# Kernel tuning notes

Hardware: AMD Instinct MI355X
Metric: run time of the kernel (lower is better)

## Reference

```python
import jax, jax.numpy as jnp
import numpy as np

C = 128        # in_channels
HEADS = 4
B, D, H, W = 4, 16, 64, 64  # H must equal W for this module's matmul to type-check


def conv1x1(x, Wm, b):
    # 1x1x1 Conv3d == per-voxel linear over channels
    return jnp.einsum('bcdhw,oc->bodhw', x, Wm) + b[None, :, None, None, None]


def setup_inputs() -> dict:
    key = jax.random.key(0)
    ks = jax.random.split(key, 14)
    scale = 1.0 / np.sqrt(C)

    def wmat(k):
        return jax.random.normal(k, (C, C), jnp.float32) * scale

    def bvec(k):
        return jax.random.normal(k, (C,), jnp.float32) * 0.01

    return {
        'x':  jax.random.normal(ks[0], (B, C, D, H, W), jnp.float32),
        'Wq': wmat(ks[1]),  'bq': bvec(ks[2]),
        'Wk': wmat(ks[3]),  'bk': bvec(ks[4]),
        'Wv': wmat(ks[5]),  'bv': bvec(ks[6]),
        'Wa1': wmat(ks[7]), 'ba1': bvec(ks[8]),
        'Wa2': wmat(ks[9]), 'ba2': bvec(ks[10]),
        'Wf': wmat(ks[11]), 'bf': bvec(ks[12]),
    }


def reference(x, Wq, bq, Wk, bk, Wv, bv, Wa1, ba1, Wa2, ba2, Wf, bf):
    b, c, d, h, w = x.shape
    ch = c // HEADS  # channels per head

    q = conv1x1(x, Wq, bq).reshape(b, HEADS, ch, d, h, w)
    k = conv1x1(x, Wk, bk).reshape(b, HEADS, ch, d, h, w)
    v = conv1x1(x, Wv, bv).reshape(b, HEADS, ch, d, h, w)

    # attention over the last spatial axis: (W, H)^T @ (H, W) -> (W, W)
    attn = jnp.einsum('bhcdxi,bhcdxj->bhcdij', q, k)  # [b, heads, ch, d, W, W]
    attn = jax.nn.softmax(attn, axis=-1)
    # (W, W) @ (H=W, W) -> (W, W)
    out = jnp.einsum('bhcdik,bhcdkj->bhcdij', attn, v)
    out = out.reshape(b, c, d, h, w)

    # depth=1 attention layer: conv1x1 -> relu -> conv1x1
    out = conv1x1(jax.nn.relu(conv1x1(out, Wa1, ba1)), Wa2, ba2)
    out = conv1x1(out, Wf, bf)
    return out
```

## Files before the change

kernel.cpp:

```cpp
#include <hip/hip_runtime.h>


#define CCH 128
#define SPB 65536
#define NBATCH 4
#define WTAB 16384
#define TSZ  16384

typedef float f32x4 __attribute__((ext_vector_type(4)));
typedef __bf16 bf16x8 __attribute__((ext_vector_type(8)));
typedef short s16x8 __attribute__((ext_vector_type(8)));
typedef unsigned short u16x8 __attribute__((ext_vector_type(8)));
typedef unsigned short u16x4 __attribute__((ext_vector_type(4)));
typedef unsigned int u32x2 __attribute__((ext_vector_type(2)));

template <typename T>
static __device__ __forceinline__ auto mfma_try(T a, T b, f32x4 c, int)
    -> decltype(__builtin_amdgcn_mfma_f32_16x16x32_bf16(a, b, c, 0, 0, 0)) {
  return __builtin_amdgcn_mfma_f32_16x16x32_bf16(a, b, c, 0, 0, 0);
}
template <typename T>
static __device__ __forceinline__ f32x4 mfma_try(T a, T b, f32x4 c, long) {
  return __builtin_amdgcn_mfma_f32_16x16x32_bf16(
      __builtin_bit_cast(bf16x8, a), __builtin_bit_cast(bf16x8, b), c, 0, 0, 0);
}
static __device__ __forceinline__ f32x4 MFMA16(u16x8 a, u16x8 b, f32x4 c) {
  return mfma_try(__builtin_bit_cast(s16x8, a), __builtin_bit_cast(s16x8, b), c, 0);
}

static __device__ __forceinline__ unsigned short f2b(float f) {
  return __builtin_bit_cast(unsigned short, (__bf16)f);
}
static __device__ __forceinline__ unsigned int pk2(float a, float b) {
  return (unsigned int)f2b(a) | ((unsigned int)f2b(b) << 16);
}

static __device__ __forceinline__ void glds16(const unsigned short* g,
                                              unsigned short* l) {
  __builtin_amdgcn_global_load_lds(
      (const __attribute__((address_space(1))) unsigned int*)g,
      (__attribute__((address_space(3))) unsigned int*)l, 16, 0, 0);
}

static __device__ __forceinline__ void bar_lgkm() {
  asm volatile("s_waitcnt lgkmcnt(0)" ::: "memory");
  __builtin_amdgcn_sched_barrier(0);
  __builtin_amdgcn_s_barrier();
  __builtin_amdgcn_sched_barrier(0);
}
static __device__ __forceinline__ void bar_vm0() {
  asm volatile("s_waitcnt vmcnt(0)" ::: "memory");
  __builtin_amdgcn_sched_barrier(0);
  __builtin_amdgcn_s_barrier();
  __builtin_amdgcn_sched_barrier(0);
}

static __device__ __forceinline__ int swzc(int r, int c) {
  int slot = ((c >> 3) ^ (r & 7) ^ ((r >> 3) & 15)) & 15;
  return r * 128 + slot * 8 + (c & 7);
}
static __device__ __forceinline__ int widx(int r, int c) {
  return (r & 64) * 128 + swzc(r & 63, c);
}
static __device__ __forceinline__ int swat(int w, int x) {
  int slot = ((x >> 3) ^ (w & 7) ^ ((w >> 3) & 7)) & 7;
  return w * 64 + slot * 8 + (x & 7);
}
static __device__ __forceinline__ int pix(int i, int j) {
  int slot = ((j >> 3) ^ (((i >> 2) & 3) << 1)) & 7;
  return i * 64 + slot * 8 + (j & 7);
}
static __device__ __forceinline__ int fdx(int o, int slot) {
  return o * 128 + ((slot ^ ((o & 7) << 2)) & 31) * 4;
}

__global__ __launch_bounds__(256) void prep_w_kernel(
    const float* __restrict__ Wq, const float* __restrict__ Wk,
    const float* __restrict__ Wv, const float* __restrict__ W1,
    const float* __restrict__ W2, const float* __restrict__ W3,
    unsigned short* __restrict__ out)
{
  const float* Ws[6] = {Wq, Wk, Wv, W1, W2, W3};
  const float* W = Ws[blockIdx.x];
  unsigned short* o = out + (size_t)blockIdx.x * WTAB;
  const int tid = threadIdx.x;
#pragma unroll
  for (int p = 0; p < 16; ++p) {
    const int base = p * 1024 + tid * 4;
    const int m = base >> 7;
    const int c0 = base & 127;
    f32x4 v = *(const f32x4*)&W[base];
    u16x4 u;
#pragma unroll
    for (int e = 0; e < 4; ++e) u[e] = f2b(v[e]);
    *(u16x4*)&o[widx(m, c0)] = u;
  }
}

__global__ __launch_bounds__(512, 2) void qkv_kernel(
    const float* __restrict__ X, const unsigned short* __restrict__ Wbf,
    const float* __restrict__ Bq, const float* __restrict__ Bk,
    const float* __restrict__ Bv,
    unsigned short* __restrict__ Yq, unsigned short* __restrict__ Yk,
    unsigned short* __restrict__ Yv)
{
  __shared__ unsigned short wt[3 * WTAB];
  __shared__ unsigned short xb[WTAB];

  const int tid  = threadIdx.x;
  const int wv   = tid >> 6;
  const int lane = tid & 63;
  const int lr   = lane & 15;
  const int lg   = lane >> 4;
  const int sw   = wv >> 2;
  const int ow   = wv & 3;
  const int lin  = blockIdx.x;
  const int swz  = ((lin & 7) << 6) | (lin >> 3);
  const int sbase = (swz & 127) * 512;
  const size_t xoff = (size_t)(swz >> 7) * CCH * SPB;
  const int go = tid * 8;

#pragma unroll
  for (int t = 0; t < 3; ++t)
#pragma unroll
    for (int p = 0; p < 4; ++p)
      glds16(&Wbf[t * WTAB + p * 4096 + go], &wt[t * WTAB + p * 4096 + go]);

  float bias_r[3][2];
#pragma unroll
  for (int of = 0; of < 2; ++of) {
    bias_r[0][of] = Bq[ow * 32 + of * 16 + lr];
    bias_r[1][of] = Bk[ow * 32 + of * 16 + lr];
    bias_r[2][of] = Bv[ow * 32 + of * 16 + lr];
  }

  const int c0  = (tid >> 3) * 2;
  const int sb8 = (tid & 7) * 4;
  const float* xrow = X + xoff + (size_t)c0 * SPB + sbase;
  unsigned int* xb32 = (unsigned int*)xb;

  f32x4 xr[8];
#pragma unroll
  for (int i = 0; i < 4; ++i) {
    xr[i]     = *(const f32x4*)&xrow[sb8 + 32 * i];
    xr[4 + i] = *(const f32x4*)&xrow[SPB + sb8 + 32 * i];
  }
#pragma unroll
  for (int i = 0; i < 4; ++i)
#pragma unroll
    for (int e = 0; e < 4; ++e)
      xb32[swzc(sb8 + 32 * i + e, c0) >> 1] = pk2(xr[i][e], xr[4 + i][e]);
  __syncthreads();

#pragma unroll
  for (int si = 0; si < 4; ++si) {
    const size_t yb =
        ((size_t)(swz >> 7) * 512 + (size_t)(swz & 127) * 4 + si) * TSZ;

    if (si < 3) {
      const float* xn = xrow + (si + 1) * 128;
#pragma unroll
      for (int i = 0; i < 4; ++i) {
        xr[i]     = *(const f32x4*)&xn[sb8 + 32 * i];
        xr[4 + i] = *(const f32x4*)&xn[SPB + sb8 + 32 * i];
      }
    }
    u16x8 afr[4][4];
#pragma unroll
    for (int sf = 0; sf < 4; ++sf)
#pragma unroll
      for (int ks = 0; ks < 4; ++ks)
        afr[sf][ks] = *(const u16x8*)
            &xb[swzc(sw * 64 + sf * 16 + lr, ks * 32 + lg * 8)];
    bar_lgkm();

    auto conv = [&](int t, unsigned short* __restrict__ Y) {
      f32x4 acc[4][2];
#pragma unroll
      for (int sf = 0; sf < 4; ++sf)
#pragma unroll
        for (int of = 0; of < 2; ++of) {
          f32x4 z = {0.f, 0.f, 0.f, 0.f};
          acc[sf][of] = z;
        }
#pragma unroll
      for (int ks = 0; ks < 4; ++ks) {
        const int k0 = ks * 32 + lg * 8;
        u16x8 w0 = *(const u16x8*)&wt[t * WTAB + widx(ow * 32 + lr, k0)];
        u16x8 w1 = *(const u16x8*)&wt[t * WTAB + widx(ow * 32 + 16 + lr, k0)];
#pragma unroll
        for (int sf = 0; sf < 4; ++sf) {
          acc[sf][0] = MFMA16(afr[sf][ks], w0, acc[sf][0]);
          acc[sf][1] = MFMA16(afr[sf][ks], w1, acc[sf][1]);
        }
      }
      const int sb = sw * 64 + lg * 4;
#pragma unroll
      for (int of = 0; of < 2; ++of) {
        const float b = bias_r[t][of];
        const size_t ob = yb + (size_t)(ow * 32 + of * 16 + lr) * 128 + sb;
#pragma unroll
        for (int sf = 0; sf < 4; ++sf) {
          u32x2 pk;
          pk.x = pk2(acc[sf][of][0] + b, acc[sf][of][1] + b);
          pk.y = pk2(acc[sf][of][2] + b, acc[sf][of][3] + b);
          *(u32x2*)&Yq[0] ;
          *(u32x2*)&Y[ob + sf * 16] = pk;
        }
      }
    };
    conv(0, Yq);
    conv(1, Yk);
    conv(2, Yv);

    if (si < 3) {
#pragma unroll
      for (int i = 0; i < 4; ++i)
#pragma unroll
        for (int e = 0; e < 4; ++e)
          xb32[swzc(sb8 + 32 * i + e, c0) >> 1] = pk2(xr[i][e], xr[4 + i][e]);
      bar_lgkm();
    }
  }
}

__global__ __launch_bounds__(256, 4) void attn64_kernel(
    const unsigned short* __restrict__ Q,
    const unsigned short* __restrict__ K,
    const unsigned short* __restrict__ V,
    unsigned short* __restrict__ O)
{
  __shared__ unsigned short qt[4096];
  __shared__ unsigned short kt[4096];
  __shared__ unsigned short vt[4096];
  __shared__ unsigned short pbuf[4096];

  const int tid  = threadIdx.x;
  const int wv   = tid >> 6;
  const int lane = tid & 63;
  const int lr   = lane & 15;
  const int lg   = lane >> 4;
  const int bid  = blockIdx.x;
  const int bs   = ((bid & 7) << 10) | (bid >> 3);
  const int b_   = bs >> 11;
  const int c_   = (bs >> 4) & 127;
  const int d_   = bs & 15;
  const size_t tb = ((size_t)b_ * 512 + (size_t)d_ * 32) * TSZ + (size_t)c_ * 128;

  {
    const int x0 = (tid >> 3) * 2;
    const int w0 = (tid & 7) * 8;
    const size_t ga = tb + (size_t)(x0 >> 1) * TSZ + w0;
    u16x8 qa = *(const u16x8*)&Q[ga], qb = *(const u16x8*)&Q[ga + 64];
    u16x8 ka = *(const u16x8*)&K[ga], kb = *(const u16x8*)&K[ga + 64];
    u16x8 va = *(const u16x8*)&V[ga], vb = *(const u16x8*)&V[ga + 64];
    unsigned int* qt32 = (unsigned int*)qt;
    unsigned int* kt32 = (unsigned int*)kt;
    unsigned int* vt32 = (unsigned int*)vt;
#pragma unroll
    for (int e = 0; e < 8; ++e) {
      const int idx = swat(w0 + e, x0) >> 1;
      qt32[idx] = (unsigned int)qa[e] | ((unsigned int)qb[e] << 16);
      kt32[idx] = (unsigned int)ka[e] | ((unsigned int)kb[e] << 16);
      vt32[idx] = (unsigned int)va[e] | ((unsigned int)vb[e] << 16);
    }
  }
  __syncthreads();

  f32x4 sacc[4];
#pragma unroll
  for (int nf = 0; nf < 4; ++nf) { f32x4 z = {0.f, 0.f, 0.f, 0.f}; sacc[nf] = z; }
#pragma unroll
  for (int ks = 0; ks < 2; ++ks) {
    const int k0 = ks * 32 + lg * 8;
    u16x8 a = *(const u16x8*)&qt[swat(wv * 16 + lr, k0)];
#pragma unroll
    for (int nf = 0; nf < 4; ++nf) {
      u16x8 bb = *(const u16x8*)&kt[swat(nf * 16 + lr, k0)];
      sacc[nf] = MFMA16(a, bb, sacc[nf]);
    }
  }

#pragma unroll
  for (int r = 0; r < 4; ++r) {
    float m = fmaxf(fmaxf(sacc[0][r], sacc[1][r]), fmaxf(sacc[2][r], sacc[3][r]));
    m = fmaxf(m, __shfl_xor(m, 1));
    m = fmaxf(m, __shfl_xor(m, 2));
    m = fmaxf(m, __shfl_xor(m, 4));
    m = fmaxf(m, __shfl_xor(m, 8));
    float sum = 0.f;
#pragma unroll
    for (int nf = 0; nf < 4; ++nf) {
      float p = __expf(sacc[nf][r] - m);
      sacc[nf][r] = p;
      sum += p;
    }
    sum += __shfl_xor(sum, 1);
    sum += __shfl_xor(sum, 2);
    sum += __shfl_xor(sum, 4);
    sum += __shfl_xor(sum, 8);
    const float inv = 1.f / sum;
    const int i = wv * 16 + lg * 4 + r;
#pragma unroll
    for (int nf = 0; nf < 4; ++nf)
      pbuf[pix(i, nf * 16 + lr)] = f2b(sacc[nf][r] * inv);
  }

  f32x4 oacc[4];
#pragma unroll
  for (int nf = 0; nf < 4; ++nf) { f32x4 z = {0.f, 0.f, 0.f, 0.f}; oacc[nf] = z; }
#pragma unroll
  for (int ks = 0; ks < 2; ++ks) {
    const int k0 = ks * 32 + lg * 8;
    u16x8 a = *(const u16x8*)&pbuf[pix(wv * 16 + lr, k0)];
#pragma unroll
    for (int nf = 0; nf < 4; ++nf) {
      u16x8 bb = *(const u16x8*)&vt[swat(nf * 16 + lr, k0)];
      oacc[nf] = MFMA16(bb, a, oacc[nf]);
    }
  }

  {
    const int i = 16 * wv + lr;
    const size_t ib = tb + (size_t)(i >> 1) * TSZ + (size_t)(i & 1) * 64 + lg * 4;
#pragma unroll
    for (int nf = 0; nf < 4; ++nf) {
      u32x2 pk;
      pk.x = pk2(oacc[nf][0], oacc[nf][1]);
      pk.y = pk2(oacc[nf][2], oacc[nf][3]);
      *(u32x2*)&O[ib + nf * 16] = pk;
    }
  }
}

__global__ __launch_bounds__(256, 2) void tail_kernel(
    const unsigned short* __restrict__ Xb, const unsigned short* __restrict__ Wbf,
    const float* __restrict__ B1, const float* __restrict__ B2,
    const float* __restrict__ B3, float* __restrict__ OUT)
{
  __shared__ unsigned short wl[16384];
  __shared__ unsigned short xc[16384];
  __shared__ float bias_lds[3][128];
  float* fA = (float*)xc;

  const int tid  = threadIdx.x;
  const int wv   = tid >> 6;
  const int lane = tid & 63;
  const int lr   = lane & 15;
  const int lg   = lane >> 4;
  const int bx   = blockIdx.x;
  const int bxs  = ((bx & 7) << 6) | (bx >> 3);
  const int s0   = bxs * 128;
  const size_t xbase = (size_t)blockIdx.y * CCH * SPB;
  const size_t tbin  = ((size_t)blockIdx.y * 512 + bxs) * TSZ;
  const int go = tid * 8;

#pragma unroll
  for (int p = 0; p < 8; ++p) glds16(&Wbf[p * 2048 + go], &wl[p * 2048 + go]);

  if (tid < 128) {
    bias_lds[0][tid] = B1[tid];
    bias_lds[1][tid] = B2[tid];
    bias_lds[2][tid] = B3[tid];
  }

  {
    const int cp = tid >> 2;
    const int sq = tid & 3;
    const unsigned short* xa = Xb + tbin + (size_t)(2 * cp) * 128 + sq * 32;
    const unsigned short* xb = xa + 128;
    unsigned int* xc32 = (unsigned int*)xc;
#pragma unroll
    for (int i = 0; i < 4; ++i) {
      u16x8 a = *(const u16x8*)&xa[8 * i];
      u16x8 b = *(const u16x8*)&xb[8 * i];
#pragma unroll
      for (int e = 0; e < 8; ++e)
        xc32[swzc(sq * 32 + 8 * i + e, 2 * cp) >> 1] =
            (unsigned int)a[e] | ((unsigned int)b[e] << 16);
    }
  }
  __syncthreads();

  u16x8 bfr[2][4];
#pragma unroll
  for (int nf = 0; nf < 2; ++nf)
#pragma unroll
    for (int ks = 0; ks < 4; ++ks)
      bfr[nf][ks] = *(const u16x8*)&xc[swzc(wv * 32 + nf * 16 + lr, ks * 32 + lg * 8)];

  f32x4 acc[8][2];
  auto gemm_std = [&]() {
#pragma unroll
    for (int mf = 0; mf < 8; ++mf)
#pragma unroll
      for (int nf = 0; nf < 2; ++nf) {
        f32x4 z = {0.f, 0.f, 0.f, 0.f};
        acc[mf][nf] = z;
      }
#pragma unroll
    for (int ks = 0; ks < 4; ++ks) {
      const int k0 = ks * 32 + lg * 8;
#pragma unroll
      for (int mf = 0; mf < 8; ++mf) {
        u16x8 afr = *(const u16x8*)&wl[widx(mf * 16 + lr, k0)];
        acc[mf][0] = MFMA16(afr, bfr[0][ks], acc[mf][0]);
        acc[mf][1] = MFMA16(afr, bfr[1][ks], acc[mf][1]);
      }
    }
  };

  auto epi_chain = [&](int ci, bool relu) {
#pragma unroll
    for (int mf = 0; mf < 8; ++mf)
#pragma unroll
      for (int nf = 0; nf < 2; ++nf) {
        const int s = wv * 32 + nf * 16 + lr;
        const int cc = mf * 16 + lg * 4;
        f32x4 bb = *(const f32x4*)&bias_lds[ci][cc];
        float v0 = acc[mf][nf][0] + bb[0];
        float v1 = acc[mf][nf][1] + bb[1];
        float v2 = acc[mf][nf][2] + bb[2];
        float v3 = acc[mf][nf][3] + bb[3];
        if (relu) {
          v0 = fmaxf(v0, 0.f); v1 = fmaxf(v1, 0.f);
          v2 = fmaxf(v2, 0.f); v3 = fmaxf(v3, 0.f);
        }
        u32x2 pk;
        pk.x = pk2(v0, v1);
        pk.y = pk2(v2, v3);
        *(u32x2*)&xc[swzc(s, cc)] = pk;
      }
#pragma unroll
    for (int nf = 0; nf < 2; ++nf)
#pragma unroll
      for (int ks = 0; ks < 4; ++ks)
        bfr[nf][ks] = *(const u16x8*)&xc[swzc(wv * 32 + nf * 16 + lr, ks * 32 + lg * 8)];
  };

#pragma unroll
  for (int j = 0; j < 2; ++j) {
    gemm_std();
    bar_lgkm();
    const unsigned short* Wn = Wbf + (size_t)(j + 1) * WTAB;
#pragma unroll
    for (int p = 0; p < 8; ++p) glds16(&Wn[p * 2048 + go], &wl[p * 2048 + go]);
    epi_chain(j, j == 0);
    bar_vm0();
  }

  {
    f32x4 acc3[2][8];
#pragma unroll
    for (int sf = 0; sf < 2; ++sf)
#pragma unroll
      for (int of = 0; of < 8; ++of) {
        f32x4 z = {0.f, 0.f, 0.f, 0.f};
        acc3[sf][of] = z;
      }
#pragma unroll
    for (int ks = 0; ks < 4; ++ks) {
      const int k0 = ks * 32 + lg * 8;
#pragma unroll
      for (int of = 0; of < 8; ++of) {
        u16x8 wfr = *(const u16x8*)&wl[widx(of * 16 + lr, k0)];
        acc3[0][of] = MFMA16(bfr[0][ks], wfr, acc3[0][of]);
        acc3[1][of] = MFMA16(bfr[1][ks], wfr, acc3[1][of]);
      }
    }

#pragma unroll
    for (int half = 0; half < 2; ++half) {
#pragma unroll
      for (int sf = 0; sf < 2; ++sf)
#pragma unroll
        for (int of4 = 0; of4 < 4; ++of4) {
          const int of = half * 4 + of4;
          const int ol = of4 * 16 + lr;
          const int slot = wv * 8 + sf * 4 + lg;
          const float b = bias_lds[2][of * 16 + lr];
          f32x4 v = acc3[sf][of];
          v[0] += b; v[1] += b; v[2] += b; v[3] += b;
          *(f32x4*)&fA[fdx(ol, slot)] = v;
        }
      bar_lgkm();
#pragma unroll
      for (int p = 0; p < 8; ++p) {
        const int r  = p * 8 + (tid >> 5);
        const int cg = tid & 31;
        f32x4 v = *(const f32x4*)&fA[fdx(r, cg)];
        *(f32x4*)&OUT[xbase + (size_t)(r + half * 64) * SPB + s0 + cg * 4] = v;
      }
      if (half == 0) bar_lgkm();
    }
  }
}

extern "C" void kernel_launch(void* const* d_in, const int* in_sizes, int n_in,
                              void* d_out, int out_size, void* d_ws, size_t ws_size,
                              hipStream_t stream) {
  const float* x   = (const float*)d_in[0];
  const float* Wq  = (const float*)d_in[1];  const float* bq  = (const float*)d_in[2];
  const float* Wk  = (const float*)d_in[3];  const float* bk  = (const float*)d_in[4];
  const float* Wv  = (const float*)d_in[5];  const float* bv  = (const float*)d_in[6];
  const float* Wa1 = (const float*)d_in[7];  const float* ba1 = (const float*)d_in[8];
  const float* Wa2 = (const float*)d_in[9];  const float* ba2 = (const float*)d_in[10];
  const float* Wf  = (const float*)d_in[11]; const float* bf_ = (const float*)d_in[12];

  unsigned short* qb  = (unsigned short*)d_ws;
  unsigned short* wbf = qb + (size_t)NBATCH * CCH * SPB;
  unsigned short* kb = (unsigned short*)d_out;
  unsigned short* vb = kb + (size_t)NBATCH * CCH * SPB;

  prep_w_kernel<<<6, 256, 0, stream>>>(Wq, Wk, Wv, Wa1, Wa2, Wf, wbf);

  qkv_kernel<<<512, 512, 0, stream>>>(x, wbf, bq, bk, bv, qb, kb, vb);

  attn64_kernel<<<NBATCH * CCH * 16, 256, 0, stream>>>(qb, kb, vb, qb);

  tail_kernel<<<dim3(SPB / 128, NBATCH), 256, 0, stream>>>(
      qb, wbf + (size_t)3 * WTAB, ba1, ba2, bf_, (float*)d_out);
}
```

Before: 189.0 us.

## Drop LDS weight staging and split QKV into one tile per block

The QKV projection kernel no longer copies all three bf16 weight tables into shared memory. Each lane now reads its weight fragments straight from global memory, relying on cache. Each block handles a single 128-voxel tile instead of looping over four with register prefetch, and the grid grows fourfold. Shared memory per block falls sharply, which should allow more resident blocks and more latency hiding. In exchange, the explicit prefetch overlap is lost and weight reads are repeated from global memory across many more blocks.

```diff
diff --git a/kernel.cpp b/kernel.cpp
--- a/kernel.cpp
+++ b/kernel.cpp
@@ -104,7 +104,6 @@
     unsigned short* __restrict__ Yq, unsigned short* __restrict__ Yk,
     unsigned short* __restrict__ Yv)
 {
-  __shared__ unsigned short wt[3 * WTAB];
   __shared__ unsigned short xb[WTAB];
 
   const int tid  = threadIdx.x;
@@ -115,16 +114,10 @@
   const int sw   = wv >> 2;
   const int ow   = wv & 3;
   const int lin  = blockIdx.x;
-  const int swz  = ((lin & 7) << 6) | (lin >> 3);
-  const int sbase = (swz & 127) * 512;
-  const size_t xoff = (size_t)(swz >> 7) * CCH * SPB;
-  const int go = tid * 8;
-
-#pragma unroll
-  for (int t = 0; t < 3; ++t)
-#pragma unroll
-    for (int p = 0; p < 4; ++p)
-      glds16(&Wbf[t * WTAB + p * 4096 + go], &wt[t * WTAB + p * 4096 + go]);
+  const int st   = ((lin & 7) << 8) | (lin >> 3);
+  const int s0   = (st & 511) * 128;
+  const size_t xoff = (size_t)(st >> 9) * CCH * SPB;
+  const size_t yb   = (size_t)st * TSZ;
 
   float bias_r[3][2];
 #pragma unroll
@@ -134,94 +127,71 @@
     bias_r[2][of] = Bv[ow * 32 + of * 16 + lr];
   }
 
-  const int c0  = (tid >> 3) * 2;
-  const int sb8 = (tid & 7) * 4;
-  const float* xrow = X + xoff + (size_t)c0 * SPB + sbase;
-  unsigned int* xb32 = (unsigned int*)xb;
-
-  f32x4 xr[8];
-#pragma unroll
-  for (int i = 0; i < 4; ++i) {
-    xr[i]     = *(const f32x4*)&xrow[sb8 + 32 * i];
-    xr[4 + i] = *(const f32x4*)&xrow[SPB + sb8 + 32 * i];
-  }
-#pragma unroll
-  for (int i = 0; i < 4; ++i)
-#pragma unroll
-    for (int e = 0; e < 4; ++e)
-      xb32[swzc(sb8 + 32 * i + e, c0) >> 1] = pk2(xr[i][e], xr[4 + i][e]);
+  {
+    const int c0  = (tid >> 3) * 2;
+    const int sb8 = (tid & 7) * 4;
+    const float* xrow = X + xoff + (size_t)c0 * SPB + s0;
+    unsigned int* xb32 = (unsigned int*)xb;
+    f32x4 xa[4], xc[4];
+#pragma unroll
+    for (int i = 0; i < 4; ++i) {
+      xa[i] = *(const f32x4*)&xrow[sb8 + 32 * i];
+      xc[i] = *(const f32x4*)&xrow[SPB + sb8 + 32 * i];
+    }
+#pragma unroll
+    for (int i = 0; i < 4; ++i)
+#pragma unroll
+      for (int e = 0; e < 4; ++e)
+        xb32[swzc(sb8 + 32 * i + e, c0) >> 1] = pk2(xa[i][e], xc[i][e]);
+  }
   __syncthreads();
 
-#pragma unroll
-  for (int si = 0; si < 4; ++si) {
-    const size_t yb =
-        ((size_t)(swz >> 7) * 512 + (size_t)(swz & 127) * 4 + si) * TSZ;
-
-    if (si < 3) {
-      const float* xn = xrow + (si + 1) * 128;
-#pragma unroll
-      for (int i = 0; i < 4; ++i) {
-        xr[i]     = *(const f32x4*)&xn[sb8 + 32 * i];
-        xr[4 + i] = *(const f32x4*)&xn[SPB + sb8 + 32 * i];
-      }
-    }
-    u16x8 afr[4][4];
+  u16x8 afr[4][4];
+#pragma unroll
+  for (int sf = 0; sf < 4; ++sf)
+#pragma unroll
+    for (int ks = 0; ks < 4; ++ks)
+      afr[sf][ks] = *(const u16x8*)
+          &xb[swzc(sw * 64 + sf * 16 + lr, ks * 32 + lg * 8)];
+
+  auto conv = [&](int t, unsigned short* __restrict__ Y) {
+    const unsigned short* Wt = Wbf + (size_t)t * WTAB;
+    f32x4 acc[4][2];
 #pragma unroll
     for (int sf = 0; sf < 4; ++sf)
 #pragma unroll
-      for (int ks = 0; ks < 4; ++ks)
-        afr[sf][ks] = *(const u16x8*)
-            &xb[swzc(sw * 64 + sf * 16 + lr, ks * 32 + lg * 8)];
-    bar_lgkm();
-
-    auto conv = [&](int t, unsigned short* __restrict__ Y) {
-      f32x4 acc[4][2];
-#pragma unroll
-      for (int sf = 0; sf < 4; ++sf)
-#pragma unroll
-        for (int of = 0; of < 2; ++of) {
-          f32x4 z = {0.f, 0.f, 0.f, 0.f};
-          acc[sf][of] = z;
-        }
-#pragma unroll
-      for (int ks = 0; ks < 4; ++ks) {
-        const int k0 = ks * 32 + lg * 8;
-        u16x8 w0 = *(const u16x8*)&wt[t * WTAB + widx(ow * 32 + lr, k0)];
-        u16x8 w1 = *(const u16x8*)&wt[t * WTAB + widx(ow * 32 + 16 + lr, k0)];
-#pragma unroll
-        for (int sf = 0; sf < 4; ++sf) {
-          acc[sf][0] = MFMA16(afr[sf][ks], w0, acc[sf][0]);
-          acc[sf][1] = MFMA16(afr[sf][ks], w1, acc[sf][1]);
-        }
-      }
-      const int sb = sw * 64 + lg * 4;
-#pragma unroll
       for (int of = 0; of < 2; ++of) {
-        const float b = bias_r[t][of];
-        const size_t ob = yb + (size_t)(ow * 32 + of * 16 + lr) * 128 + sb;
-#pragma unroll
-        for (int sf = 0; sf < 4; ++sf) {
-          u32x2 pk;
-          pk.x = pk2(acc[sf][of][0] + b, acc[sf][of][1] + b);
-          pk.y = pk2(acc[sf][of][2] + b, acc[sf][of][3] + b);
-          *(u32x2*)&Yq[0] ;
-          *(u32x2*)&Y[ob + sf * 16] = pk;
-        }
-      }
-    };
-    conv(0, Yq);
-    conv(1, Yk);
-    conv(2, Yv);
-
-    if (si < 3) {
-#pragma unroll
-      for (int i = 0; i < 4; ++i)
-#pragma unroll
-        for (int e = 0; e < 4; ++e)
-          xb32[swzc(sb8 + 32 * i + e, c0) >> 1] = pk2(xr[i][e], xr[4 + i][e]);
-      bar_lgkm();
-    }
-  }
+        f32x4 z = {0.f, 0.f, 0.f, 0.f};
+        acc[sf][of] = z;
+      }
+#pragma unroll
+    for (int ks = 0; ks < 4; ++ks) {
+      const int k0 = ks * 32 + lg * 8;
+      u16x8 w0 = *(const u16x8*)&Wt[widx(ow * 32 + lr, k0)];
+      u16x8 w1 = *(const u16x8*)&Wt[widx(ow * 32 + 16 + lr, k0)];
+#pragma unroll
+      for (int sf = 0; sf < 4; ++sf) {
+        acc[sf][0] = MFMA16(afr[sf][ks], w0, acc[sf][0]);
+        acc[sf][1] = MFMA16(afr[sf][ks], w1, acc[sf][1]);
+      }
+    }
+    const int sb = sw * 64 + lg * 4;
+#pragma unroll
+    for (int of = 0; of < 2; ++of) {
+      const float b = bias_r[t][of];
+      const size_t ob = yb + (size_t)(ow * 32 + of * 16 + lr) * 128 + sb;
+#pragma unroll
+      for (int sf = 0; sf < 4; ++sf) {
+        u32x2 pk;
+        pk.x = pk2(acc[sf][of][0] + b, acc[sf][of][1] + b);
+        pk.y = pk2(acc[sf][of][2] + b, acc[sf][of][3] + b);
+        *(u32x2*)&Y[ob + sf * 16] = pk;
+      }
+    }
+  };
+  conv(0, Yq);
+  conv(1, Yk);
+  conv(2, Yv);
 }
 
 __global__ __launch_bounds__(256, 4) void attn64_kernel(
@@ -514,7 +484,7 @@
 
   prep_w_kernel<<<6, 256, 0, stream>>>(Wq, Wk, Wv, Wa1, Wa2, Wf, wbf);
 
-  qkv_kernel<<<512, 512, 0, stream>>>(x, wbf, bq, bk, bv, qb, kb, vb);
+  qkv_kernel<<<2048, 512, 0, stream>>>(x, wbf, bq, bk, bv, qb, kb, vb);
 
   attn64_kernel<<<NBATCH * CCH * 16, 256, 0, stream>>>(qb, kb, vb, qb);
 
```

Measured after the change: 212.8 us. +12.6%, slower.
